# Kernel tuning notes

Hardware: AMD Instinct MI355X
Metric: run time of the kernel (lower is better)

## Reference

```python
import jax, jax.numpy as jnp
import numpy as np
from math import sqrt

B, P, D = 4, 2048, 1024
H, DK = 16, 64  # n_heads, d_keys


def setup_inputs() -> dict:
    key = jax.random.key(0)
    ks = jax.random.split(key, 6)
    s = 1.0 / sqrt(D)
    return {
        "target_embedding": jax.random.normal(ks[0], (B, P, D), dtype=jnp.float32),
        "Wq": jax.random.normal(ks[1], (D, H * DK), dtype=jnp.float32) * s,
        "bq": jnp.zeros((H * DK,), dtype=jnp.float32),
        "Wk": jax.random.normal(ks[2], (D, H * DK), dtype=jnp.float32) * s,
        "bk": jnp.zeros((H * DK,), dtype=jnp.float32),
        "Wv": jax.random.normal(ks[3], (D, H * DK), dtype=jnp.float32) * s,
        "bv": jnp.zeros((H * DK,), dtype=jnp.float32),
        "Wo": jax.random.normal(ks[4], (H * DK, D), dtype=jnp.float32) * s,
        "bo": jnp.zeros((D,), dtype=jnp.float32),
    }


def reference(target_embedding, Wq, bq, Wk, bk, Wv, bv, Wo, bo):
    x = target_embedding
    b, p, _ = x.shape
    # QKV projections -> [B, P, H, DK]
    q = (x @ Wq + bq).reshape(b, p, H, DK)
    k = (x @ Wk + bk).reshape(b, p, H, DK)
    v = (x @ Wv + bv).reshape(b, p, H, DK)
    scale = 1.0 / sqrt(DK)
    scores = jnp.einsum("bphd,bqhd->bhpq", q, k)  # [B, H, P, P]
    A = jax.nn.softmax(scale * scores, axis=-1)  # dropout is identity in eval
    rep = jnp.einsum("bhpq,bqhd->bphd", A, v).reshape(b, p, H * DK)
    return rep @ Wo + bo
```

## Files before the change

kernel.cpp:

```cpp
#include <hip/hip_runtime.h>

typedef __attribute__((ext_vector_type(8))) short short8;
typedef __attribute__((ext_vector_type(4))) float f32x4;
typedef __attribute__((ext_vector_type(4))) unsigned short ushort4v;

#define GLOBAL_AS __attribute__((address_space(1)))
#define LDS_AS    __attribute__((address_space(3)))

__device__ __forceinline__ unsigned short f2bf(float f) {
    unsigned int u = __float_as_uint(f);
    u += 0x7fffu + ((u >> 16) & 1u);
    return (unsigned short)(u >> 16);
}

__device__ __forceinline__ float fexp2(float x) {
    return __builtin_amdgcn_exp2f(x);
}

__device__ __forceinline__ void async_cp16(void* lds, const void* g) {
    __builtin_amdgcn_global_load_lds((GLOBAL_AS unsigned int*)g,
                                     (LDS_AS unsigned int*)lds, 16, 0, 0);
}

#define SCL2E 0.18033688011112042591999058512524f

__global__ void convert_x_kernel(const float* __restrict__ X,
                                 unsigned short* __restrict__ Xb) {
    int i = (blockIdx.x * 256 + threadIdx.x) * 4;
    float4 v = *(const float4*)&X[i];
    ushort4v o;
    o.x = f2bf(v.x); o.y = f2bf(v.y); o.z = f2bf(v.z); o.w = f2bf(v.w);
    *(ushort4v*)&Xb[i] = o;
}

__global__ void transpose_w_kernel(const float* __restrict__ Wq,
                                   const float* __restrict__ Wk,
                                   const float* __restrict__ Wv,
                                   const float* __restrict__ Wo,
                                   unsigned short* __restrict__ Wts) {
    __shared__ float tile[32][33];
    const int z = blockIdx.z;
    const float* src = (z == 0) ? Wq : (z == 1) ? Wk : (z == 2) ? Wv : Wo;
    unsigned short* dst = Wts + z * 1048576;
    const int tx = threadIdx.x, ty = threadIdx.y;
    const int x0 = blockIdx.x * 32, y0 = blockIdx.y * 32;
#pragma unroll
    for (int i = 0; i < 32; i += 8)
        tile[ty + i][tx] = src[(y0 + ty + i) * 1024 + x0 + tx];
    __syncthreads();
#pragma unroll
    for (int i = 0; i < 32; i += 8)
        dst[(x0 + ty + i) * 1024 + y0 + tx] = f2bf(tile[tx][ty + i]);
}

__device__ __forceinline__ void gemm_mainloop_128(
    const unsigned short* __restrict__ A, const unsigned short* __restrict__ Bt,
    int m0, int n0, unsigned short* As, unsigned short* Bs, f32x4 acc[4][4]) {
    const int tid = threadIdx.x;
    const int lane = tid & 63;
    const int wave = tid >> 6;
    const int wr = wave >> 1, wc = wave & 1;
    const int c = lane & 15, quad = lane >> 4;

#pragma unroll
    for (int mt = 0; mt < 4; ++mt)
#pragma unroll
        for (int nt = 0; nt < 4; ++nt)
            acc[mt][nt] = (f32x4)0.0f;

    for (int k0 = 0; k0 < 1024; k0 += 32) {
#pragma unroll
        for (int i = 0; i < 2; ++i) {
            int s = tid + 256 * i;
            int r = s >> 2, gp = s & 3;
            int g = gp ^ ((r >> 1) & 3);
            async_cp16(&As[s * 8], &A[(m0 + r) * 1024 + k0 + g * 8]);
        }
#pragma unroll
        for (int i = 0; i < 2; ++i) {
            int s = tid + 256 * i;
            int r = s >> 2, gp = s & 3;
            int g = gp ^ ((r >> 1) & 3);
            async_cp16(&Bs[s * 8], &Bt[(n0 + r) * 1024 + k0 + g * 8]);
        }
        asm volatile("s_waitcnt vmcnt(0)" ::: "memory");
        __syncthreads();

        short8 af[4], bf[4];
#pragma unroll
        for (int mt = 0; mt < 4; ++mt) {
            int r = wr * 64 + mt * 16 + c;
            int gp = quad ^ ((r >> 1) & 3);
            af[mt] = *(const short8*)&As[r * 32 + gp * 8];
        }
#pragma unroll
        for (int nt = 0; nt < 4; ++nt) {
            int r = wc * 64 + nt * 16 + c;
            int gp = quad ^ ((r >> 1) & 3);
            bf[nt] = *(const short8*)&Bs[r * 32 + gp * 8];
        }
#pragma unroll
        for (int mt = 0; mt < 4; ++mt)
#pragma unroll
            for (int nt = 0; nt < 4; ++nt)
                acc[mt][nt] = __builtin_amdgcn_mfma_f32_16x16x32_bf16(
                    af[mt], bf[nt], acc[mt][nt], 0, 0, 0);
        __syncthreads();
    }
}

__global__ __launch_bounds__(256, 3) void gemm_qkv_kernel(
    const unsigned short* __restrict__ Xb, const unsigned short* __restrict__ Wts,
    const float* __restrict__ bq, const float* __restrict__ bk,
    const float* __restrict__ bv, unsigned short* __restrict__ Qb,
    unsigned short* __restrict__ Kb, unsigned short* __restrict__ Vtb) {
    __shared__ __align__(16) unsigned short As[128 * 32];
    __shared__ __align__(16) unsigned short Bs[128 * 32];
    const int z = blockIdx.z;
    const unsigned short* Bt = Wts + z * 1048576;
    const float* bias = (z == 0) ? bq : (z == 1) ? bk : bv;
    const int m0 = blockIdx.y * 128, n0 = blockIdx.x * 128;
    f32x4 acc[4][4];
    gemm_mainloop_128(Xb, Bt, m0, n0, As, Bs, acc);

    const int lane = threadIdx.x & 63, wave = threadIdx.x >> 6;
    const int wr = wave >> 1, wc = wave & 1;
    const int c = lane & 15, quad = lane >> 4;
    unsigned short* dstQK = (z == 0) ? Qb : Kb;
    const float qscale = (z == 0) ? SCL2E : 1.0f;
#pragma unroll
    for (int nt = 0; nt < 4; ++nt) {
        int col = n0 + wc * 64 + nt * 16 + c;
        float bb = bias[col];
        int h = col >> 6, dk = col & 63;
#pragma unroll
        for (int mt = 0; mt < 4; ++mt) {
#pragma unroll
            for (int r = 0; r < 4; ++r) {
                int row = m0 + wr * 64 + mt * 16 + quad * 4 + r;
                int b = row >> 11, p = row & 2047;
                float v = (acc[mt][nt][r] + bb) * qscale;
                if (z < 2)
                    dstQK[((b * 16 + h) * 2048 + p) * 64 + dk] = f2bf(v);
                else
                    Vtb[((b * 16 + h) * 64 + dk) * 2048 + p] = f2bf(v);
            }
        }
    }
}

__global__ __launch_bounds__(256, 4) void attn_kernel(
    const unsigned short* __restrict__ Q, const unsigned short* __restrict__ K,
    const unsigned short* __restrict__ Vt, unsigned short* __restrict__ rep) {
    __shared__ __align__(16) unsigned short Ks[64 * 64];
    __shared__ __align__(16) unsigned short Vs[64 * 64];
    __shared__ __align__(16) unsigned short Ps[4][32 * 72];
    const int tid = threadIdx.x, lane = tid & 63, wave = tid >> 6;
    const int c = lane & 15, quad = lane >> 4;
    const int bh = blockIdx.y;
    const int q0 = blockIdx.x * 128 + wave * 32;
    const unsigned short* Qbh = Q + bh * (2048 * 64);
    const unsigned short* Kbh = K + bh * (2048 * 64);
    const unsigned short* Vbh = Vt + bh * (64 * 2048);

    short8 qf[2][2];
#pragma unroll
    for (int t = 0; t < 2; ++t)
#pragma unroll
        for (int ks = 0; ks < 2; ++ks)
            qf[t][ks] = *(const short8*)&Qbh[(q0 + t * 16 + c) * 64 + ks * 32 + quad * 8];

    f32x4 o[2][4];
    float lpart[2][4];
#pragma unroll
    for (int t = 0; t < 2; ++t) {
#pragma unroll
        for (int d = 0; d < 4; ++d) o[t][d] = (f32x4)0.0f;
#pragma unroll
        for (int r = 0; r < 4; ++r) lpart[t][r] = 0.0f;
    }

    for (int k0 = 0; k0 < 2048; k0 += 64) {
#pragma unroll
        for (int i = 0; i < 2; ++i) {
            int s = tid + 256 * i;
            int r = s >> 3, gp = s & 7;
            int g = gp ^ (r & 7);
            async_cp16(&Ks[s * 8], &Kbh[(k0 + r) * 64 + g * 8]);
        }
#pragma unroll
        for (int i = 0; i < 2; ++i) {
            int s = tid + 256 * i;
            int r = s >> 3, gp = s & 7;
            int g = gp ^ (r & 7);
            async_cp16(&Vs[s * 8], &Vbh[r * 2048 + k0 + g * 8]);
        }
        asm volatile("s_waitcnt vmcnt(0)" ::: "memory");
        __syncthreads();

        short8 kf[4][2];
#pragma unroll
        for (int nt = 0; nt < 4; ++nt)
#pragma unroll
            for (int ks = 0; ks < 2; ++ks) {
                int r = nt * 16 + c;
                int gp2 = (quad + 4 * ks) ^ (r & 7);
                kf[nt][ks] = *(const short8*)&Ks[r * 64 + gp2 * 8];
            }

        f32x4 sc[2][4];
#pragma unroll
        for (int t = 0; t < 2; ++t)
#pragma unroll
            for (int nt = 0; nt < 4; ++nt) {
                f32x4 z4 = (f32x4)0.0f;
                z4 = __builtin_amdgcn_mfma_f32_16x16x32_bf16(qf[t][0], kf[nt][0], z4, 0, 0, 0);
                sc[t][nt] = __builtin_amdgcn_mfma_f32_16x16x32_bf16(qf[t][1], kf[nt][1], z4, 0, 0, 0);
            }

#pragma unroll
        for (int t = 0; t < 2; ++t)
#pragma unroll
            for (int nt = 0; nt < 4; ++nt)
#pragma unroll
                for (int r = 0; r < 4; ++r) {
                    float p = fexp2(sc[t][nt][r]);
                    lpart[t][r] += p;
                    Ps[wave][(t * 16 + quad * 4 + r) * 72 + nt * 16 + c] = f2bf(p);
                }
        asm volatile("s_waitcnt lgkmcnt(0)" ::: "memory");

        short8 pf[2][2];
#pragma unroll
        for (int t = 0; t < 2; ++t)
#pragma unroll
            for (int ks = 0; ks < 2; ++ks)
                pf[t][ks] = *(const short8*)&Ps[wave][(t * 16 + c) * 72 + ks * 32 + quad * 8];
#pragma unroll
        for (int dkt = 0; dkt < 4; ++dkt) {
#pragma unroll
            for (int ks = 0; ks < 2; ++ks) {
                int r = dkt * 16 + c;
                int gp2 = (quad + 4 * ks) ^ (r & 7);
                short8 vf = *(const short8*)&Vs[r * 64 + gp2 * 8];
#pragma unroll
                for (int t = 0; t < 2; ++t)
                    o[t][dkt] = __builtin_amdgcn_mfma_f32_16x16x32_bf16(
                        pf[t][ks], vf, o[t][dkt], 0, 0, 0);
            }
        }
        __syncthreads();
    }

    const int b = bh >> 4, h = bh & 15;
#pragma unroll
    for (int t = 0; t < 2; ++t) {
        float inv[4];
#pragma unroll
        for (int r = 0; r < 4; ++r) {
            float l = lpart[t][r];
            l += __shfl_xor(l, 1);
            l += __shfl_xor(l, 2);
            l += __shfl_xor(l, 4);
            l += __shfl_xor(l, 8);
            inv[r] = 1.0f / l;
        }
#pragma unroll
        for (int dkt = 0; dkt < 4; ++dkt)
#pragma unroll
            for (int r = 0; r < 4; ++r)
                rep[(b * 2048 + q0 + t * 16 + quad * 4 + r) * 1024 + h * 64 + dkt * 16 + c] =
                    f2bf(o[t][dkt][r] * inv[r]);
    }
}

__global__ __launch_bounds__(256, 3) void gemm_out_kernel(
    const unsigned short* __restrict__ rep, const unsigned short* __restrict__ Wot,
    const float* __restrict__ bo, float* __restrict__ out) {
    __shared__ __align__(16) unsigned short As[128 * 32];
    __shared__ __align__(16) unsigned short Bs[128 * 32];
    const int m0 = blockIdx.y * 128, n0 = blockIdx.x * 128;
    f32x4 acc[4][4];
    gemm_mainloop_128(rep, Wot, m0, n0, As, Bs, acc);
    const int lane = threadIdx.x & 63, wave = threadIdx.x >> 6;
    const int wr = wave >> 1, wc = wave & 1;
    const int c = lane & 15, quad = lane >> 4;
#pragma unroll
    for (int nt = 0; nt < 4; ++nt) {
        int col = n0 + wc * 64 + nt * 16 + c;
        float bb = bo[col];
#pragma unroll
        for (int mt = 0; mt < 4; ++mt) {
            int row = m0 + wr * 64 + mt * 16 + quad * 4;
#pragma unroll
            for (int r = 0; r < 4; ++r)
                out[(row + r) * 1024 + col] = acc[mt][nt][r] + bb;
        }
    }
}

extern "C" void kernel_launch(void* const* d_in, const int* in_sizes, int n_in,
                              void* d_out, int out_size, void* d_ws, size_t ws_size,
                              hipStream_t stream) {
    (void)in_sizes; (void)n_in; (void)out_size; (void)ws_size;
    const float* X  = (const float*)d_in[0];
    const float* Wq = (const float*)d_in[1];
    const float* bq = (const float*)d_in[2];
    const float* Wk = (const float*)d_in[3];
    const float* bk = (const float*)d_in[4];
    const float* Wv = (const float*)d_in[5];
    const float* bv = (const float*)d_in[6];
    const float* Wo = (const float*)d_in[7];
    const float* bo = (const float*)d_in[8];
    float* out = (float*)d_out;

    char* ws = (char*)d_ws;
    unsigned short* Xb   = (unsigned short*)(ws);
    unsigned short* Wts  = (unsigned short*)(ws + (16u << 20));
    unsigned short* Qb   = (unsigned short*)(ws + (24u << 20));
    unsigned short* Kb   = (unsigned short*)(ws + (40u << 20));
    unsigned short* Vtb  = (unsigned short*)(ws + (56u << 20));
    unsigned short* repb = (unsigned short*)(ws);

    convert_x_kernel<<<8192, 256, 0, stream>>>(X, Xb);
    transpose_w_kernel<<<dim3(32, 32, 4), dim3(32, 8), 0, stream>>>(Wq, Wk, Wv, Wo, Wts);
    gemm_qkv_kernel<<<dim3(8, 64, 3), 256, 0, stream>>>(Xb, Wts, bq, bk, bv, Qb, Kb, Vtb);
    attn_kernel<<<dim3(16, 64), 256, 0, stream>>>(Qb, Kb, Vtb, repb);
    gemm_out_kernel<<<dim3(8, 64), 256, 0, stream>>>(repb, Wts + 3 * 1048576, bo, out);
}
```

Before: 321.3 us.

## Double-buffer K/V tiles in attention via register prefetch; transpose V separately

The attention loop now loads the next K/V tile into registers while computing on the current one. Tiles are stored into one of two LDS buffers, which drops one barrier per iteration and the global-to-LDS async copies. The QKV GEMM now writes V in row layout, and a new transpose kernel produces the Vt layout, replacing the strided scattered stores in the GEMM epilogue. In exchange this adds an extra kernel launch and a V round trip through memory, doubles LDS use, and lowers the occupancy hint from 4 to 3.

```diff
diff --git a/kernel.cpp b/kernel.cpp
--- a/kernel.cpp
+++ b/kernel.cpp
@@ -53,6 +53,23 @@
         dst[(x0 + ty + i) * 1024 + y0 + tx] = f2bf(tile[tx][ty + i]);
 }
 
+__global__ void transpose_v_kernel(const unsigned short* __restrict__ V,
+                                   unsigned short* __restrict__ Vt) {
+    __shared__ unsigned short tile[32][33];
+    const int bh = blockIdx.z;
+    const int p0 = blockIdx.x * 32, d0 = blockIdx.y * 32;
+    const unsigned short* src = V + bh * (2048 * 64);
+    unsigned short* dst = Vt + bh * (2048 * 64);
+    const int tx = threadIdx.x, ty = threadIdx.y;
+#pragma unroll
+    for (int i = 0; i < 32; i += 8)
+        tile[ty + i][tx] = src[(p0 + ty + i) * 64 + d0 + tx];
+    __syncthreads();
+#pragma unroll
+    for (int i = 0; i < 32; i += 8)
+        dst[(d0 + ty + i) * 2048 + p0 + tx] = tile[tx][ty + i];
+}
+
 __device__ __forceinline__ void gemm_mainloop_128(
     const unsigned short* __restrict__ A, const unsigned short* __restrict__ Bt,
     int m0, int n0, unsigned short* As, unsigned short* Bs, f32x4 acc[4][4]) {
@@ -113,7 +130,7 @@
     const unsigned short* __restrict__ Xb, const unsigned short* __restrict__ Wts,
     const float* __restrict__ bq, const float* __restrict__ bk,
     const float* __restrict__ bv, unsigned short* __restrict__ Qb,
-    unsigned short* __restrict__ Kb, unsigned short* __restrict__ Vtb) {
+    unsigned short* __restrict__ Kb, unsigned short* __restrict__ Vb) {
     __shared__ __align__(16) unsigned short As[128 * 32];
     __shared__ __align__(16) unsigned short Bs[128 * 32];
     const int z = blockIdx.z;
@@ -126,7 +143,7 @@
     const int lane = threadIdx.x & 63, wave = threadIdx.x >> 6;
     const int wr = wave >> 1, wc = wave & 1;
     const int c = lane & 15, quad = lane >> 4;
-    unsigned short* dstQK = (z == 0) ? Qb : Kb;
+    unsigned short* dst = (z == 0) ? Qb : (z == 1) ? Kb : Vb;
     const float qscale = (z == 0) ? SCL2E : 1.0f;
 #pragma unroll
     for (int nt = 0; nt < 4; ++nt) {
@@ -140,20 +157,30 @@
                 int row = m0 + wr * 64 + mt * 16 + quad * 4 + r;
                 int b = row >> 11, p = row & 2047;
                 float v = (acc[mt][nt][r] + bb) * qscale;
-                if (z < 2)
-                    dstQK[((b * 16 + h) * 2048 + p) * 64 + dk] = f2bf(v);
-                else
-                    Vtb[((b * 16 + h) * 64 + dk) * 2048 + p] = f2bf(v);
+                dst[((b * 16 + h) * 2048 + p) * 64 + dk] = f2bf(v);
             }
         }
     }
 }
 
-__global__ __launch_bounds__(256, 4) void attn_kernel(
+__device__ __forceinline__ void load_kv_regs(
+    const unsigned short* __restrict__ Kbh, const unsigned short* __restrict__ Vbh,
+    int k0, int tid, short8 kr[2], short8 vr[2]) {
+#pragma unroll
+    for (int i = 0; i < 2; ++i) {
+        int s = tid + 256 * i;
+        int r = s >> 3, gp = s & 7;
+        int g = gp ^ (r & 7);
+        kr[i] = *(const short8*)&Kbh[(k0 + r) * 64 + g * 8];
+        vr[i] = *(const short8*)&Vbh[r * 2048 + k0 + g * 8];
+    }
+}
+
+__global__ __launch_bounds__(256, 3) void attn_kernel(
     const unsigned short* __restrict__ Q, const unsigned short* __restrict__ K,
     const unsigned short* __restrict__ Vt, unsigned short* __restrict__ rep) {
-    __shared__ __align__(16) unsigned short Ks[64 * 64];
-    __shared__ __align__(16) unsigned short Vs[64 * 64];
+    __shared__ __align__(16) unsigned short Ks[2][64 * 64];
+    __shared__ __align__(16) unsigned short Vs[2][64 * 64];
     __shared__ __align__(16) unsigned short Ps[4][32 * 72];
     const int tid = threadIdx.x, lane = tid & 63, wave = tid >> 6;
     const int c = lane & 15, quad = lane >> 4;
@@ -170,6 +197,9 @@
         for (int ks = 0; ks < 2; ++ks)
             qf[t][ks] = *(const short8*)&Qbh[(q0 + t * 16 + c) * 64 + ks * 32 + quad * 8];
 
+    short8 kr[2], vr[2];
+    load_kv_regs(Kbh, Vbh, 0, tid, kr, vr);
+
     f32x4 o[2][4];
     float lpart[2][4];
 #pragma unroll
@@ -180,23 +210,20 @@
         for (int r = 0; r < 4; ++r) lpart[t][r] = 0.0f;
     }
 
-    for (int k0 = 0; k0 < 2048; k0 += 64) {
+#pragma unroll 2
+    for (int it = 0; it < 32; ++it) {
+        const int buf = it & 1;
+        unsigned short* Ksb = &Ks[buf][0];
+        unsigned short* Vsb = &Vs[buf][0];
 #pragma unroll
         for (int i = 0; i < 2; ++i) {
             int s = tid + 256 * i;
-            int r = s >> 3, gp = s & 7;
-            int g = gp ^ (r & 7);
-            async_cp16(&Ks[s * 8], &Kbh[(k0 + r) * 64 + g * 8]);
-        }
-#pragma unroll
-        for (int i = 0; i < 2; ++i) {
-            int s = tid + 256 * i;
-            int r = s >> 3, gp = s & 7;
-            int g = gp ^ (r & 7);
-            async_cp16(&Vs[s * 8], &Vbh[r * 2048 + k0 + g * 8]);
-        }
-        asm volatile("s_waitcnt vmcnt(0)" ::: "memory");
+            *(short8*)&Ksb[s * 8] = kr[i];
+            *(short8*)&Vsb[s * 8] = vr[i];
+        }
         __syncthreads();
+        if (it < 31)
+            load_kv_regs(Kbh, Vbh, (it + 1) * 64, tid, kr, vr);
 
         short8 kf[4][2];
 #pragma unroll
@@ -205,7 +232,7 @@
             for (int ks = 0; ks < 2; ++ks) {
                 int r = nt * 16 + c;
                 int gp2 = (quad + 4 * ks) ^ (r & 7);
-                kf[nt][ks] = *(const short8*)&Ks[r * 64 + gp2 * 8];
+                kf[nt][ks] = *(const short8*)&Ksb[r * 64 + gp2 * 8];
             }
 
         f32x4 sc[2][4];
@@ -242,14 +269,13 @@
             for (int ks = 0; ks < 2; ++ks) {
                 int r = dkt * 16 + c;
                 int gp2 = (quad + 4 * ks) ^ (r & 7);
-                short8 vf = *(const short8*)&Vs[r * 64 + gp2 * 8];
+                short8 vf = *(const short8*)&Vsb[r * 64 + gp2 * 8];
 #pragma unroll
                 for (int t = 0; t < 2; ++t)
                     o[t][dkt] = __builtin_amdgcn_mfma_f32_16x16x32_bf16(
                         pf[t][ks], vf, o[t][dkt], 0, 0, 0);
             }
         }
-        __syncthreads();
     }
 
     const int b = bh >> 4, h = bh & 15;
@@ -319,12 +345,14 @@
     unsigned short* Wts  = (unsigned short*)(ws + (16u << 20));
     unsigned short* Qb   = (unsigned short*)(ws + (24u << 20));
     unsigned short* Kb   = (unsigned short*)(ws + (40u << 20));
-    unsigned short* Vtb  = (unsigned short*)(ws + (56u << 20));
-    unsigned short* repb = (unsigned short*)(ws);
+    unsigned short* Vb   = (unsigned short*)(ws + (56u << 20));
+    unsigned short* Vtb  = (unsigned short*)(ws);
+    unsigned short* repb = (unsigned short*)(ws + (56u << 20));
 
     convert_x_kernel<<<8192, 256, 0, stream>>>(X, Xb);
     transpose_w_kernel<<<dim3(32, 32, 4), dim3(32, 8), 0, stream>>>(Wq, Wk, Wv, Wo, Wts);
-    gemm_qkv_kernel<<<dim3(8, 64, 3), 256, 0, stream>>>(Xb, Wts, bq, bk, bv, Qb, Kb, Vtb);
+    gemm_qkv_kernel<<<dim3(8, 64, 3), 256, 0, stream>>>(Xb, Wts, bq, bk, bv, Qb, Kb, Vb);
+    transpose_v_kernel<<<dim3(64, 2, 64), dim3(32, 8), 0, stream>>>(Vb, Vtb);
     attn_kernel<<<dim3(16, 64), 256, 0, stream>>>(Qb, Kb, Vtb, repb);
     gemm_out_kernel<<<dim3(8, 64), 256, 0, stream>>>(repb, Wts + 3 * 1048576, bo, out);
 }
```

Result: faster. 308.7 us (-3.9%).
